# Kernel optimization log

Hardware: AMD Instinct MI355X
Metric: run time of the kernel (lower is better)

The kernel has to match this reference:

```python
import jax, jax.numpy as jnp
import numpy as np

T = 48  # top-T from init

def setup_inputs() -> dict:
    key = jax.random.key(0)
    ks = jax.random.split(key, 8)
    B, C, H, W = 16, 512, 32, 32
    tc = C // 8
    return {
        "x": jax.random.normal(ks[0], (B, C, H, W), jnp.float32),
        "fW": jax.random.normal(ks[1], (tc, C), jnp.float32) * 0.05,
        "fb": jax.random.normal(ks[2], (tc,), jnp.float32) * 0.05,
        "gW": jax.random.normal(ks[3], (tc, C), jnp.float32) * 0.05,
        "gb": jax.random.normal(ks[4], (tc,), jnp.float32) * 0.05,
        "hW": jax.random.normal(ks[5], (C, C), jnp.float32) * 0.05,
        "hb": jax.random.normal(ks[6], (C,), jnp.float32) * 0.05,
        "scale": jax.random.normal(ks[7], (1,), jnp.float32),
    }

def reference(x, fW, fb, gW, gb, hW, hb, scale):
    B, C, H, W = x.shape
    tc = fW.shape[0]
    HW = H * W
    # normalize by Frobenius norm over (batch, channel) -> [H, W]
    xn = x / jnp.linalg.norm(x, axis=(0, 1))[None, None]  # [B,C,H,W]
    # 1x1 convs, output already channel-last [B,H,W,out]
    f = jnp.einsum('bchw,oc->bhwo', xn, fW) + fb          # [B,H,W,tc]
    g = jnp.einsum('bchw,oc->bhwo', xn, gW) + gb          # [B,H,W,tc]
    h = jnp.einsum('bchw,oc->bhwo', xn, hW) + hb          # [B,H,W,C]
    xp = jnp.transpose(xn, (0, 2, 3, 1))                  # [B,H,W,C]
    # scores: queries H-major, keys W-major (faithful to permute(0,3,2,1).reshape)
    g_keys = jnp.transpose(g, (0, 3, 2, 1)).reshape(B, tc, HW)  # [B,tc,W*H]
    s = jnp.matmul(f.reshape(B, HW, tc), g_keys)          # [B,HW,HW]
    beta = jax.nn.softmax(s, axis=-1)
    o = jnp.matmul(beta, h.reshape(B, HW, C)).reshape(B, H, W, C)
    fdd = scale * o + xp                                  # [B,H,W,C]
    # per-batch correlation: fdd[b] ([H,W,C]) @ fdd[b].reshape(C,HW)
    corr = jnp.einsum('bhwc,bcn->bhwn', fdd, fdd.reshape(B, C, HW))  # [B,H,W,HW]
    top = jax.lax.top_k(corr, T)[0]                       # descending top-T values
    top = jax.nn.relu(top)
    top = top / jnp.linalg.norm(top, axis=(0, 1))[None, None]  # norm over (B,H) -> [W,T]
    return jnp.transpose(top, (0, 3, 1, 2))               # [B,T,H,W]
```

## Files before the change

### kernel.cpp

```cpp
#include <hip/hip_runtime.h>
#include <cstdint>
#include <cstddef>

#define B_   16
#define C_   512
#define H_   32
#define W_   32
#define HW_  1024
#define TC_  64
#define T_   48

typedef unsigned short u16;
typedef __attribute__((ext_vector_type(8))) short short8v;
typedef __attribute__((ext_vector_type(4))) float f32x4;

__device__ __forceinline__ u16 tobf(float x) {
    unsigned u = __float_as_uint(x);
    return (u16)((u + 0x7FFFu + ((u >> 16) & 1u)) >> 16);
}
__device__ __forceinline__ float frombf(u16 h) {
    return __uint_as_float(((unsigned)h) << 16);
}

__device__ __forceinline__ void gld16(const void* g, void* l) {
    __builtin_amdgcn_global_load_lds(
        (const __attribute__((address_space(1))) void*)g,
        (__attribute__((address_space(3))) void*)l, 16, 0, 0);
}

__global__ void k_colsq(const float* __restrict__ x, float* __restrict__ partial) {
    int bid = blockIdx.x;
    int col = (bid & 3) * 256 + threadIdx.x;
    int r0  = (bid >> 2) * 128;
    const float* p = x + (size_t)r0 * HW_ + col;
    float s = 0.f;
    for (int r = 0; r < 128; ++r) { float v = p[(size_t)r * HW_]; s += v * v; }
    partial[(size_t)(bid >> 2) * HW_ + col] = s;
}

__global__ void k_rsqrt(const float* __restrict__ partial, float* __restrict__ ninv) {
    int i = blockIdx.x * 256 + threadIdx.x;
    if (i < HW_) {
        float s = 0.f;
        for (int r = 0; r < 64; ++r) s += partial[(size_t)r * HW_ + i];
        ninv[i] = rsqrtf(s);
    }
}

__global__ void k_transpose(const float* __restrict__ x, const float* __restrict__ ninv,
                            u16* __restrict__ obH) {
    __shared__ float tile[32][33];
    int b  = blockIdx.z;
    int m0 = blockIdx.x * 32, c0 = blockIdx.y * 32;
    int tx = threadIdx.x, ty = threadIdx.y;
    const float* xb = x + (size_t)b * C_ * HW_;
    #pragma unroll
    for (int j = 0; j < 32; j += 8)
        tile[ty + j][tx] = xb[(size_t)(c0 + ty + j) * HW_ + m0 + tx];
    __syncthreads();
    size_t base = (size_t)b * HW_ * C_;
    #pragma unroll
    for (int j = 0; j < 32; j += 8) {
        int m = m0 + ty + j;
        obH[base + (size_t)m * C_ + c0 + tx] = tobf(tile[tx][ty + j] * ninv[m]);
    }
}

__global__ void k_packW(const float* __restrict__ in, u16* __restrict__ oh) {
    size_t i = (size_t)blockIdx.x * 256 + threadIdx.x;
    oh[i] = tobf(in[i]);
}
__global__ void k_packFG(const float* __restrict__ fW, const float* __restrict__ gW,
                         const float* __restrict__ fb, const float* __restrict__ gb,
                         u16* __restrict__ oh, float* __restrict__ fgb) {
    int idx = blockIdx.x * 256 + threadIdx.x;
    int row = idx >> 9, c = idx & 511;
    float v = (row < 64) ? fW[row * 512 + c] : gW[(row - 64) * 512 + c];
    oh[idx] = tobf(v);
    if (idx < 128) fgb[idx] = (idx < 64) ? fb[idx] : gb[idx - 64];
}

template<int PERMB, int EPI>
__global__ __launch_bounds__(256) void k_gemm1(
    const u16* __restrict__ A, const u16* __restrict__ Bm,
    const float* __restrict__ bias,
    float* __restrict__ Cf, u16* __restrict__ Ch,
    const float* __restrict__ scaleP,
    int N, int K, int lda, int ldb, long sA, long sB, long sC)
{
    __shared__ u16 lds[3 * 8192];
    const int b = blockIdx.z;
    const u16* pA = A + (size_t)b * sA;
    const u16* pB = Bm + (size_t)b * sB;
    const int m0 = blockIdx.y * 128, n0 = blockIdx.x * 128;
    const int tid = threadIdx.x, wave = tid >> 6, lane = tid & 63;
    const int wm = wave >> 1, wn = wave & 1;
    const int g = lane >> 4;

    f32x4 acc[4][4];
    #pragma unroll
    for (int i = 0; i < 4; ++i)
        #pragma unroll
        for (int j = 0; j < 4; ++j) { f32x4 z = {0.f,0.f,0.f,0.f}; acc[i][j] = z; }

    auto STAGE = [&](int kt, int buf) {
        const int k0 = kt << 5;
        u16* lb = lds + buf * 8192;
        #pragma unroll
        for (int q = 0; q < 4; ++q) {
            int ci = wave * 4 + q;
            bool isA = ci < 8;
            int li = ci & 7;
            const u16* gp = isA ? pA : pB;
            int ld = isA ? lda : ldb;
            int rb = isA ? m0 : n0;
            int rp = li * 8 + (lane >> 3);
            int gg = (lane & 7) ^ (rp & 7);
            int r  = rp * 2 + (gg >> 2);
            int kc = k0 + (gg & 3) * 8;
            int rowg = rb + r;
            if (PERMB && !isA) rowg = ((rowg & 31) << 5) | (rowg >> 5);
            gld16(gp + (size_t)rowg * ld + kc,
                  lb + (isA ? 0 : 4096) + li * 512 + lane * 8);
        }
    };
    auto COMPUTE = [&](int buf) {
        const u16* As = lds + buf * 8192;
        const u16* Bs = As + 4096;
        short8v av[4];
        #pragma unroll
        for (int i = 0; i < 4; ++i) {
            int r = wm * 64 + i * 16 + (lane & 15);
            int rp = r >> 1, gg = ((r & 1) << 2) + g;
            av[i] = *(const short8v*)(As + rp * 64 + ((gg ^ (rp & 7)) << 3));
        }
        #pragma unroll
        for (int j = 0; j < 4; ++j) {
            int r = wn * 64 + j * 16 + (lane & 15);
            int rp = r >> 1, gg = ((r & 1) << 2) + g;
            short8v bv = *(const short8v*)(Bs + rp * 64 + ((gg ^ (rp & 7)) << 3));
            #pragma unroll
            for (int i = 0; i < 4; ++i)
                acc[i][j] = __builtin_amdgcn_mfma_f32_16x16x32_bf16(av[i], bv, acc[i][j], 0, 0, 0);
        }
    };

    const int nkt = K >> 5;
    STAGE(0, 0);
    STAGE(1, 1);
    int cur = 0;
    for (int kt = 0; kt < nkt; ++kt) {
        int nxt2 = cur + 2; if (nxt2 >= 3) nxt2 -= 3;
        if (kt + 2 < nkt) {
            STAGE(kt + 2, nxt2);
            asm volatile("s_waitcnt vmcnt(8)" ::: "memory");
        } else if (kt + 1 < nkt) {
            asm volatile("s_waitcnt vmcnt(4)" ::: "memory");
        } else {
            asm volatile("s_waitcnt vmcnt(0)" ::: "memory");
        }
        __builtin_amdgcn_s_barrier();
        __builtin_amdgcn_sched_barrier(0);
        COMPUTE(cur);
        __builtin_amdgcn_sched_barrier(0);
        __builtin_amdgcn_s_barrier();
        ++cur; if (cur >= 3) cur -= 3;
    }

    const float sc = (EPI == 2) ? scaleP[0] : 0.f;
    const int colbase = n0 + wn * 64 + (lane & 15);
    const int rowbase = m0 + wm * 64 + ((lane >> 4) << 2);
    #pragma unroll
    for (int i = 0; i < 4; ++i)
        #pragma unroll
        for (int j = 0; j < 4; ++j) {
            int col = colbase + j * 16;
            #pragma unroll
            for (int rg = 0; rg < 4; ++rg) {
                int row = rowbase + i * 16 + rg;
                size_t idx = (size_t)b * sC + (size_t)row * N + col;
                float a = acc[i][j][rg];
                if (EPI == 0)      Cf[idx] = a;
                else if (EPI == 2) Ch[idx] = tobf(sc * a + frombf(Ch[idx]));
                else if (EPI == 4) Ch[idx] = tobf(a);
                else if (EPI == 5) Ch[idx] = tobf(a + bias[row]);
                else               Ch[idx] = tobf(a + bias[col]);
            }
        }
}

template<int PERMB, int EPI>
__global__ __launch_bounds__(512) void k_gemm2(
    const u16* __restrict__ A, const u16* __restrict__ Bm,
    const float* __restrict__ bias,
    float* __restrict__ Cf, u16* __restrict__ Ch,
    const float* __restrict__ scaleP,
    int N, int K, int lda, int ldb, long sA, long sB, long sC)
{
    __shared__ u16 lds[3 * 12288];
    const int b = blockIdx.z;
    const u16* pA = A + (size_t)b * sA;
    const u16* pB = Bm + (size_t)b * sB;
    const int m0 = blockIdx.y * 128, n0 = blockIdx.x * 256;
    const int tid = threadIdx.x, wave = tid >> 6, lane = tid & 63;
    const int wm = wave >> 2, wn = wave & 3;
    const int g = lane >> 4;

    f32x4 acc[4][4];
    #pragma unroll
    for (int i = 0; i < 4; ++i)
        #pragma unroll
        for (int j = 0; j < 4; ++j) { f32x4 z = {0.f,0.f,0.f,0.f}; acc[i][j] = z; }

    auto STAGE = [&](int kt, int buf) {
        const int k0 = kt << 5;
        u16* lb = lds + buf * 12288;
        #pragma unroll
        for (int q = 0; q < 3; ++q) {
            int ci = wave * 3 + q;
            bool isA = ci < 8;
            int li = isA ? ci : ci - 8;
            const u16* gp = isA ? pA : pB;
            int ld = isA ? lda : ldb;
            int rb = isA ? m0 : n0;
            int rp = li * 8 + (lane >> 3);
            int gg = (lane & 7) ^ (rp & 7);
            int r  = rp * 2 + (gg >> 2);
            int kc = k0 + (gg & 3) * 8;
            int rowg = rb + r;
            if (PERMB && !isA) rowg = ((rowg & 31) << 5) | (rowg >> 5);
            gld16(gp + (size_t)rowg * ld + kc,
                  lb + (isA ? 0 : 4096) + li * 512 + lane * 8);
        }
    };
    auto COMPUTE = [&](int buf) {
        const u16* As = lds + buf * 12288;
        const u16* Bs = As + 4096;
        short8v av[4];
        #pragma unroll
        for (int i = 0; i < 4; ++i) {
            int r = wm * 64 + i * 16 + (lane & 15);
            int rp = r >> 1, gg = ((r & 1) << 2) + g;
            av[i] = *(const short8v*)(As + rp * 64 + ((gg ^ (rp & 7)) << 3));
        }
        #pragma unroll
        for (int j = 0; j < 4; ++j) {
            int r = wn * 64 + j * 16 + (lane & 15);
            int rp = r >> 1, gg = ((r & 1) << 2) + g;
            short8v bv = *(const short8v*)(Bs + rp * 64 + ((gg ^ (rp & 7)) << 3));
            #pragma unroll
            for (int i = 0; i < 4; ++i)
                acc[i][j] = __builtin_amdgcn_mfma_f32_16x16x32_bf16(av[i], bv, acc[i][j], 0, 0, 0);
        }
    };

    const int nkt = K >> 5;
    STAGE(0, 0);
    STAGE(1, 1);
    int cur = 0;
    for (int kt = 0; kt < nkt; ++kt) {
        int nxt2 = cur + 2; if (nxt2 >= 3) nxt2 -= 3;
        if (kt + 2 < nkt) {
            STAGE(kt + 2, nxt2);
            asm volatile("s_waitcnt vmcnt(6)" ::: "memory");
        } else if (kt + 1 < nkt) {
            asm volatile("s_waitcnt vmcnt(3)" ::: "memory");
        } else {
            asm volatile("s_waitcnt vmcnt(0)" ::: "memory");
        }
        __builtin_amdgcn_s_barrier();
        __builtin_amdgcn_sched_barrier(0);
        COMPUTE(cur);
        __builtin_amdgcn_sched_barrier(0);
        __builtin_amdgcn_s_barrier();
        ++cur; if (cur >= 3) cur -= 3;
    }

    const float sc = (EPI == 2) ? scaleP[0] : 0.f;
    const int colbase = n0 + wn * 64 + (lane & 15);
    const int rowbase = m0 + wm * 64 + ((lane >> 4) << 2);
    #pragma unroll
    for (int i = 0; i < 4; ++i)
        #pragma unroll
        for (int j = 0; j < 4; ++j) {
            int col = colbase + j * 16;
            #pragma unroll
            for (int rg = 0; rg < 4; ++rg) {
                int row = rowbase + i * 16 + rg;
                size_t idx = (size_t)b * sC + (size_t)row * N + col;
                float a = acc[i][j][rg];
                if (EPI == 0)      Cf[idx] = a;
                else if (EPI == 2) Ch[idx] = tobf(sc * a + frombf(Ch[idx]));
                else if (EPI == 4) Ch[idx] = tobf(a);
                else if (EPI == 5) Ch[idx] = tobf(a + bias[row]);
                else               Ch[idx] = tobf(a + bias[col]);
            }
        }
}

__global__ __launch_bounds__(256) void k_softmax(u16* __restrict__ S) {
    size_t row = blockIdx.x;
    u16* r = S + row * (size_t)HW_;
    int t = threadIdx.x;
    ushort4 raw = ((const ushort4*)r)[t];
    float v0 = frombf(raw.x), v1 = frombf(raw.y), v2 = frombf(raw.z), v3 = frombf(raw.w);

    __shared__ float redm[4], reds[4];
    int wid = t >> 6, lane = t & 63;

    float m = fmaxf(fmaxf(v0, v1), fmaxf(v2, v3));
    for (int o = 32; o > 0; o >>= 1) m = fmaxf(m, __shfl_down(m, o));
    if (lane == 0) redm[wid] = m;
    __syncthreads();
    if (t == 0) redm[0] = fmaxf(fmaxf(redm[0], redm[1]), fmaxf(redm[2], redm[3]));
    __syncthreads();
    m = redm[0];

    v0 = expf(v0 - m); v1 = expf(v1 - m); v2 = expf(v2 - m); v3 = expf(v3 - m);
    float s = v0 + v1 + v2 + v3;
    for (int o = 32; o > 0; o >>= 1) s += __shfl_down(s, o);
    if (lane == 0) reds[wid] = s;
    __syncthreads();
    if (t == 0) reds[0] = reds[0] + reds[1] + reds[2] + reds[3];
    __syncthreads();
    float inv = 1.f / reds[0];
    ushort4 o4;
    o4.x = tobf(v0 * inv); o4.y = tobf(v1 * inv);
    o4.z = tobf(v2 * inv); o4.w = tobf(v3 * inv);
    ((ushort4*)r)[t] = o4;
}

__global__ void k_tposeU1(const u16* __restrict__ src, u16* __restrict__ dst) {
    __shared__ u16 tile[32][33];
    int b = blockIdx.z;
    const u16* sb = src + (size_t)b * (C_ * HW_);
    u16* db = dst + (size_t)b * (C_ * HW_);
    int c0 = blockIdx.x * 32, r0 = blockIdx.y * 32;
    int tx = threadIdx.x, ty = threadIdx.y;
    #pragma unroll
    for (int j = 0; j < 32; j += 8)
        tile[ty + j][tx] = sb[(size_t)(r0 + ty + j) * HW_ + c0 + tx];
    __syncthreads();
    #pragma unroll
    for (int j = 0; j < 32; j += 8)
        db[(size_t)(c0 + ty + j) * C_ + r0 + tx] = tile[tx][ty + j];
}

__device__ __forceinline__ float sort64_desc(float v, int lane) {
    #pragma unroll
    for (int k = 2; k <= 64; k <<= 1) {
        #pragma unroll
        for (int j = k >> 1; j > 0; j >>= 1) {
            float o = __shfl_xor(v, j);
            bool takeMax = (((lane & k) == 0) == ((lane & j) == 0));
            v = takeMax ? fmaxf(v, o) : fminf(v, o);
        }
    }
    return v;
}
__device__ __forceinline__ float bmerge64_desc(float a, float b, int lane) {
    float br = __shfl(b, 63 - lane);
    float c = fmaxf(a, br);
    #pragma unroll
    for (int j = 32; j > 0; j >>= 1) {
        float o = __shfl_xor(c, j);
        c = ((lane & j) == 0) ? fmaxf(c, o) : fminf(c, o);
    }
    return c;
}

__global__ __launch_bounds__(256) void k_topk(const float* __restrict__ corr,
                                              float* __restrict__ topv) {
    __shared__ float buf[4][1024];
    int wave = threadIdx.x >> 6, lane = threadIdx.x & 63;
    int row = blockIdx.x * 4 + wave;
    const float4* rp = (const float4*)(corr + (size_t)row * HW_);

    float4 e[4];
    #pragma unroll
    for (int q = 0; q < 4; ++q) e[q] = rp[lane * 4 + q];

    float gm = -INFINITY;
    #pragma unroll
    for (int q = 0; q < 4; ++q)
        gm = fmaxf(gm, fmaxf(fmaxf(e[q].x, e[q].y), fmaxf(e[q].z, e[q].w)));
    float sorted = sort64_desc(gm, lane);
    float tau = __shfl(sorted, T_ - 1);

    int c = 0;
    #pragma unroll
    for (int q = 0; q < 4; ++q)
        c += (e[q].x >= tau) + (e[q].y >= tau) + (e[q].z >= tau) + (e[q].w >= tau);
    int sc = c;
    #pragma unroll
    for (int o = 1; o < 64; o <<= 1) {
        int t2 = __shfl_up(sc, o);
        if (lane >= o) sc += t2;
    }
    int off = sc - c;
    int cnt = __shfl(sc, 63);

    float* wb = buf[wave];
    #pragma unroll
    for (int q = 0; q < 4; ++q) {
        if (e[q].x >= tau) wb[off++] = e[q].x;
        if (e[q].y >= tau) wb[off++] = e[q].y;
        if (e[q].z >= tau) wb[off++] = e[q].z;
        if (e[q].w >= tau) wb[off++] = e[q].w;
    }

    float* orow = topv + (size_t)row * T_;
    if (cnt <= 64) {
        float a = (lane < cnt) ? wb[lane] : -INFINITY;
        a = sort64_desc(a, lane);
        if (lane < T_) orow[lane] = fmaxf(a, 0.f);
    } else if (cnt <= 128) {
        float a  = sort64_desc(wb[lane], lane);
        float b2 = sort64_desc((lane < cnt - 64) ? wb[64 + lane] : -INFINITY, lane);
        float m2 = bmerge64_desc(a, b2, lane);
        if (lane < T_) orow[lane] = fmaxf(m2, 0.f);
    } else {
        int P = 256; while (P < cnt) P <<= 1;
        for (int i = cnt + lane; i < P; i += 64) wb[i] = -INFINITY;
        for (int k = 2; k <= P; k <<= 1)
            for (int j = k >> 1; j > 0; j >>= 1)
                for (int t2 = lane; t2 < P; t2 += 64) {
                    int ixj = t2 ^ j;
                    if (ixj > t2) {
                        float a = wb[t2], b3 = wb[ixj];
                        bool desc = ((t2 & k) == 0);
                        if (desc ? (a < b3) : (a > b3)) { wb[t2] = b3; wb[ixj] = a; }
                    }
                }
        if (lane < T_) orow[lane] = fmaxf(wb[lane], 0.f);
    }
}

__global__ void k_colss(const float* __restrict__ topv, float* __restrict__ colss) {
    int o = blockIdx.x;
    int w = o / T_, t = o % T_;
    int lane = threadIdx.x;
    float s = 0.f;
    for (int i = lane; i < 512; i += 64) {
        int b = i >> 5, h = i & 31;
        float v = topv[(size_t)((b << 10) + (h << 5) + w) * T_ + t];
        s += v * v;
    }
    for (int off = 32; off > 0; off >>= 1) s += __shfl_down(s, off);
    if (lane == 0) colss[o] = s;
}

__global__ void k_final(const float* __restrict__ topv, const float* __restrict__ colss,
                        float* __restrict__ out) {
    int idx = blockIdx.x * 256 + threadIdx.x;
    if (idx >= B_ * T_ * HW_) return;
    int w = idx & 31;
    int h = (idx >> 5) & 31;
    int t = (idx >> 10) % T_;
    int b = idx / (T_ * HW_);
    float v = topv[(size_t)((b << 10) + (h << 5) + w) * T_ + t];
    out[idx] = v * rsqrtf(colss[w * T_ + t]);
}

extern "C" void kernel_launch(void* const* d_in, const int* in_sizes, int n_in,
                              void* d_out, int out_size, void* d_ws, size_t ws_size,
                              hipStream_t stream) {
    const float* x     = (const float*)d_in[0];
    const float* fW    = (const float*)d_in[1];
    const float* fb    = (const float*)d_in[2];
    const float* gW    = (const float*)d_in[3];
    const float* gb    = (const float*)d_in[4];
    const float* hW    = (const float*)d_in[5];
    const float* hb    = (const float*)d_in[6];
    const float* scale = (const float*)d_in[7];
    float* out = (float*)d_out;

    char* wsb = (char*)d_ws;
    float* part = (float*)(wsb + 0);
    float* ninv = (float*)(wsb + 262144);
    u16*   hWh  = (u16*)(wsb + 266240);
    u16*   fgWh = (u16*)(wsb + 790528);
    float* fgb  = (float*)(wsb + 921600);
    u16*   xnH  = (u16*)(wsb + 922112);
    u16*   fgH  = (u16*)(wsb + 17699328);
    u16*   fgL  = (u16*)(wsb + 21893632);
    u16*   hvTH = (u16*)(wsb + 26087936);
    float* S    = (float*)(wsb + 42865152);
    float* topv = (float*)fgH;
    float* colss= (float*)fgL;
    u16*   Sp   = (u16*)S;

    const long sXn = 524288;
    const long sFG = 131072;
    const long sS  = 1048576;

    k_colsq<<<256, 256, 0, stream>>>(x, part);
    k_rsqrt<<<4, 256, 0, stream>>>(part, ninv);

    k_transpose<<<dim3(32, 16, 16), dim3(32, 8), 0, stream>>>(x, ninv, xnH);

    k_packW<<<1024, 256, 0, stream>>>(hW, hWh);
    k_packFG<<<256, 256, 0, stream>>>(fW, gW, fb, gb, fgWh, fgb);

    k_gemm1<0, 6><<<dim3(1, 8, 16), 256, 0, stream>>>(
        xnH, fgWh, fgb, nullptr, fgH, nullptr,
        128, 512, 512, 512, sXn, 0, sFG);

    k_gemm1<0, 5><<<dim3(8, 4, 16), 256, 0, stream>>>(
        hWh, xnH, hb, nullptr, hvTH, nullptr,
        1024, 512, 512, 512, 0, sXn, sXn);

    k_gemm2<1, 4><<<dim3(4, 8, 16), 512, 0, stream>>>(
        fgH, fgH + 64, nullptr, nullptr, Sp, nullptr,
        1024, 64, 128, 128, sFG, sFG, sS);

    k_softmax<<<B_ * HW_, 256, 0, stream>>>(Sp);

    k_gemm1<0, 2><<<dim3(4, 8, 16), 256, 0, stream>>>(
        Sp, hvTH, nullptr, nullptr, xnH, scale,
        512, 1024, 1024, 1024, sS, sXn, sXn);

    k_tposeU1<<<dim3(32, 16, 16), dim3(32, 8), 0, stream>>>(xnH, hvTH);

    k_gemm1<0, 0><<<dim3(8, 8, 16), 256, 0, stream>>>(
        xnH, hvTH, nullptr, S, nullptr, nullptr,
        1024, 512, 512, 512, sXn, sXn, sS);

    k_topk<<<B_ * HW_ / 4, 256, 0, stream>>>(S, topv);

    k_colss<<<W_ * T_, 64, 0, stream>>>(topv, colss);
    k_final<<<(B_ * T_ * HW_ + 255) / 256, 256, 0, stream>>>(topv, colss, out);
}
```

Before: 215.4 us.

## Fuse score GEMM with row softmax and swizzle GEMM block order

Replaces the separate score GEMM plus softmax kernel with one kernel. Each block computes a 64x1024 tile of scores with MFMA, does the row max and sum reductions in registers and shared memory, and writes normalized bf16 probabilities through a swizzled LDS staging buffer. This removes the bf16 score round trip to global memory and one launch. The score logits are also no longer rounded to bf16 before softmax. Separately, k_gemm1 remaps block IDs in a stride-8 interleave, likely meant to spread blocks across XCDs and improve cache locality. The fused kernel uses about 136KB of LDS, which caps occupancy at one block per CU.

```diff
diff --git a/kernel.cpp b/kernel.cpp
--- a/kernel.cpp
+++ b/kernel.cpp
@@ -80,7 +80,7 @@
     if (idx < 128) fgb[idx] = (idx < 64) ? fb[idx] : gb[idx - 64];
 }
 
-template<int PERMB, int EPI>
+template<int EPI>
 __global__ __launch_bounds__(256) void k_gemm1(
     const u16* __restrict__ A, const u16* __restrict__ Bm,
     const float* __restrict__ bias,
@@ -89,10 +89,18 @@
     int N, int K, int lda, int ldb, long sA, long sB, long sC)
 {
     __shared__ u16 lds[3 * 8192];
-    const int b = blockIdx.z;
+    const int gx = gridDim.x, gy = gridDim.y, gz = gridDim.z;
+    int bidl = blockIdx.x + gx * (blockIdx.y + gy * blockIdx.z);
+    int nwg = gx * gy * gz;
+    int sw = (bidl & 7) * (nwg >> 3) + (bidl >> 3);
+    int gxy = gx * gy;
+    int bz = sw / gxy, rem = sw - bz * gxy;
+    int by = rem / gx, bx = rem - by * gx;
+
+    const int b = bz;
     const u16* pA = A + (size_t)b * sA;
     const u16* pB = Bm + (size_t)b * sB;
-    const int m0 = blockIdx.y * 128, n0 = blockIdx.x * 128;
+    const int m0 = by * 128, n0 = bx * 128;
     const int tid = threadIdx.x, wave = tid >> 6, lane = tid & 63;
     const int wm = wave >> 1, wn = wave & 1;
     const int g = lane >> 4;
@@ -118,9 +126,7 @@
             int gg = (lane & 7) ^ (rp & 7);
             int r  = rp * 2 + (gg >> 2);
             int kc = k0 + (gg & 3) * 8;
-            int rowg = rb + r;
-            if (PERMB && !isA) rowg = ((rowg & 31) << 5) | (rowg >> 5);
-            gld16(gp + (size_t)rowg * ld + kc,
+            gld16(gp + (size_t)(rb + r) * ld + kc,
                   lb + (isA ? 0 : 4096) + li * 512 + lane * 8);
         }
     };
@@ -182,152 +188,175 @@
                 float a = acc[i][j][rg];
                 if (EPI == 0)      Cf[idx] = a;
                 else if (EPI == 2) Ch[idx] = tobf(sc * a + frombf(Ch[idx]));
-                else if (EPI == 4) Ch[idx] = tobf(a);
                 else if (EPI == 5) Ch[idx] = tobf(a + bias[row]);
                 else               Ch[idx] = tobf(a + bias[col]);
             }
         }
 }
 
-template<int PERMB, int EPI>
-__global__ __launch_bounds__(512) void k_gemm2(
-    const u16* __restrict__ A, const u16* __restrict__ Bm,
-    const float* __restrict__ bias,
-    float* __restrict__ Cf, u16* __restrict__ Ch,
-    const float* __restrict__ scaleP,
-    int N, int K, int lda, int ldb, long sA, long sB, long sC)
+__global__ __launch_bounds__(512) void k_ssoft(
+    const u16* __restrict__ fg,
+    u16* __restrict__ P)
 {
-    __shared__ u16 lds[3 * 12288];
-    const int b = blockIdx.z;
-    const u16* pA = A + (size_t)b * sA;
-    const u16* pB = Bm + (size_t)b * sB;
-    const int m0 = blockIdx.y * 128, n0 = blockIdx.x * 256;
+    __shared__ u16 lds[69632];
+    __shared__ float red[512];
+    __shared__ float rowm[64];
+    __shared__ float rinv[64];
+
+    const int b = blockIdx.y;
+    const int m0 = blockIdx.x * 64;
+    const u16* fgb = fg + (size_t)b * 131072;
     const int tid = threadIdx.x, wave = tid >> 6, lane = tid & 63;
-    const int wm = wave >> 2, wn = wave & 3;
+    const int wn = wave;
     const int g = lane >> 4;
 
-    f32x4 acc[4][4];
-    #pragma unroll
-    for (int i = 0; i < 4; ++i)
-        #pragma unroll
-        for (int j = 0; j < 4; ++j) { f32x4 z = {0.f,0.f,0.f,0.f}; acc[i][j] = z; }
-
-    auto STAGE = [&](int kt, int buf) {
-        const int k0 = kt << 5;
-        u16* lb = lds + buf * 12288;
-        #pragma unroll
-        for (int q = 0; q < 3; ++q) {
-            int ci = wave * 3 + q;
-            bool isA = ci < 8;
-            int li = isA ? ci : ci - 8;
-            const u16* gp = isA ? pA : pB;
-            int ld = isA ? lda : ldb;
-            int rb = isA ? m0 : n0;
+    #pragma unroll
+    for (int kc = 0; kc < 2; ++kc) {
+        #pragma unroll
+        for (int q = 0; q < 8; ++q) {
+            int li = wave * 8 + q;
             int rp = li * 8 + (lane >> 3);
             int gg = (lane & 7) ^ (rp & 7);
             int r  = rp * 2 + (gg >> 2);
-            int kc = k0 + (gg & 3) * 8;
-            int rowg = rb + r;
-            if (PERMB && !isA) rowg = ((rowg & 31) << 5) | (rowg >> 5);
-            gld16(gp + (size_t)rowg * ld + kc,
-                  lb + (isA ? 0 : 4096) + li * 512 + lane * 8);
-        }
-    };
-    auto COMPUTE = [&](int buf) {
-        const u16* As = lds + buf * 12288;
-        const u16* Bs = As + 4096;
+            int n2 = ((r & 31) << 5) | (r >> 5);
+            int kcol = 64 + kc * 32 + (gg & 3) * 8;
+            gld16(fgb + (size_t)n2 * 128 + kcol,
+                  lds + 4096 + kc * 32768 + li * 512 + lane * 8);
+        }
+        if (lane < 32) {
+            int rp = wave * 4 + (lane >> 3);
+            int gg = (lane & 7) ^ (rp & 7);
+            int r  = rp * 2 + (gg >> 2);
+            int kcol = kc * 32 + (gg & 3) * 8;
+            gld16(fgb + (size_t)(m0 + r) * 128 + kcol,
+                  lds + kc * 2048 + wave * 256 + lane * 8);
+        }
+    }
+    __syncthreads();
+
+    f32x4 acc[4][8];
+    #pragma unroll
+    for (int i = 0; i < 4; ++i)
+        #pragma unroll
+        for (int j = 0; j < 8; ++j) { f32x4 z = {0.f,0.f,0.f,0.f}; acc[i][j] = z; }
+
+    #pragma unroll
+    for (int kc = 0; kc < 2; ++kc) {
+        const u16* As = lds + kc * 2048;
+        const u16* Bs = lds + 4096 + kc * 32768;
         short8v av[4];
         #pragma unroll
         for (int i = 0; i < 4; ++i) {
-            int r = wm * 64 + i * 16 + (lane & 15);
+            int r = i * 16 + (lane & 15);
             int rp = r >> 1, gg = ((r & 1) << 2) + g;
             av[i] = *(const short8v*)(As + rp * 64 + ((gg ^ (rp & 7)) << 3));
         }
         #pragma unroll
-        for (int j = 0; j < 4; ++j) {
-            int r = wn * 64 + j * 16 + (lane & 15);
-            int rp = r >> 1, gg = ((r & 1) << 2) + g;
+        for (int j = 0; j < 8; ++j) {
+            int n = wn * 128 + j * 16 + (lane & 15);
+            int rp = n >> 1, gg = ((n & 1) << 2) + g;
             short8v bv = *(const short8v*)(Bs + rp * 64 + ((gg ^ (rp & 7)) << 3));
             #pragma unroll
             for (int i = 0; i < 4; ++i)
                 acc[i][j] = __builtin_amdgcn_mfma_f32_16x16x32_bf16(av[i], bv, acc[i][j], 0, 0, 0);
         }
-    };
-
-    const int nkt = K >> 5;
-    STAGE(0, 0);
-    STAGE(1, 1);
-    int cur = 0;
-    for (int kt = 0; kt < nkt; ++kt) {
-        int nxt2 = cur + 2; if (nxt2 >= 3) nxt2 -= 3;
-        if (kt + 2 < nkt) {
-            STAGE(kt + 2, nxt2);
-            asm volatile("s_waitcnt vmcnt(6)" ::: "memory");
-        } else if (kt + 1 < nkt) {
-            asm volatile("s_waitcnt vmcnt(3)" ::: "memory");
-        } else {
-            asm volatile("s_waitcnt vmcnt(0)" ::: "memory");
-        }
-        __builtin_amdgcn_s_barrier();
-        __builtin_amdgcn_sched_barrier(0);
-        COMPUTE(cur);
-        __builtin_amdgcn_sched_barrier(0);
-        __builtin_amdgcn_s_barrier();
-        ++cur; if (cur >= 3) cur -= 3;
-    }
-
-    const float sc = (EPI == 2) ? scaleP[0] : 0.f;
-    const int colbase = n0 + wn * 64 + (lane & 15);
-    const int rowbase = m0 + wm * 64 + ((lane >> 4) << 2);
+    }
+
+    const int rgrp = (lane >> 4) << 2;
+    float pm[4][4];
     #pragma unroll
     for (int i = 0; i < 4; ++i)
         #pragma unroll
-        for (int j = 0; j < 4; ++j) {
-            int col = colbase + j * 16;
-            #pragma unroll
-            for (int rg = 0; rg < 4; ++rg) {
-                int row = rowbase + i * 16 + rg;
-                size_t idx = (size_t)b * sC + (size_t)row * N + col;
-                float a = acc[i][j][rg];
-                if (EPI == 0)      Cf[idx] = a;
-                else if (EPI == 2) Ch[idx] = tobf(sc * a + frombf(Ch[idx]));
-                else if (EPI == 4) Ch[idx] = tobf(a);
-                else if (EPI == 5) Ch[idx] = tobf(a + bias[row]);
-                else               Ch[idx] = tobf(a + bias[col]);
+        for (int rg = 0; rg < 4; ++rg) {
+            float m = acc[i][0][rg];
+            #pragma unroll
+            for (int j = 1; j < 8; ++j) m = fmaxf(m, acc[i][j][rg]);
+            pm[i][rg] = m;
+        }
+    #pragma unroll
+    for (int o = 1; o < 16; o <<= 1)
+        #pragma unroll
+        for (int i = 0; i < 4; ++i)
+            #pragma unroll
+            for (int rg = 0; rg < 4; ++rg)
+                pm[i][rg] = fmaxf(pm[i][rg], __shfl_xor(pm[i][rg], o));
+    if ((lane & 15) == 0)
+        #pragma unroll
+        for (int i = 0; i < 4; ++i)
+            #pragma unroll
+            for (int rg = 0; rg < 4; ++rg)
+                red[wn * 64 + i * 16 + rgrp + rg] = pm[i][rg];
+    __syncthreads();
+    if (tid < 64) {
+        float m = red[tid];
+        #pragma unroll
+        for (int w = 1; w < 8; ++w) m = fmaxf(m, red[w * 64 + tid]);
+        rowm[tid] = m;
+    }
+    __syncthreads();
+
+    float ps[4][4];
+    #pragma unroll
+    for (int i = 0; i < 4; ++i)
+        #pragma unroll
+        for (int rg = 0; rg < 4; ++rg) {
+            float m = rowm[i * 16 + rgrp + rg];
+            float s = 0.f;
+            #pragma unroll
+            for (int j = 0; j < 8; ++j) {
+                float e = expf(acc[i][j][rg] - m);
+                acc[i][j][rg] = e;
+                s += e;
             }
-        }
-}
-
-__global__ __launch_bounds__(256) void k_softmax(u16* __restrict__ S) {
-    size_t row = blockIdx.x;
-    u16* r = S + row * (size_t)HW_;
-    int t = threadIdx.x;
-    ushort4 raw = ((const ushort4*)r)[t];
-    float v0 = frombf(raw.x), v1 = frombf(raw.y), v2 = frombf(raw.z), v3 = frombf(raw.w);
-
-    __shared__ float redm[4], reds[4];
-    int wid = t >> 6, lane = t & 63;
-
-    float m = fmaxf(fmaxf(v0, v1), fmaxf(v2, v3));
-    for (int o = 32; o > 0; o >>= 1) m = fmaxf(m, __shfl_down(m, o));
-    if (lane == 0) redm[wid] = m;
-    __syncthreads();
-    if (t == 0) redm[0] = fmaxf(fmaxf(redm[0], redm[1]), fmaxf(redm[2], redm[3]));
-    __syncthreads();
-    m = redm[0];
-
-    v0 = expf(v0 - m); v1 = expf(v1 - m); v2 = expf(v2 - m); v3 = expf(v3 - m);
-    float s = v0 + v1 + v2 + v3;
-    for (int o = 32; o > 0; o >>= 1) s += __shfl_down(s, o);
-    if (lane == 0) reds[wid] = s;
-    __syncthreads();
-    if (t == 0) reds[0] = reds[0] + reds[1] + reds[2] + reds[3];
-    __syncthreads();
-    float inv = 1.f / reds[0];
-    ushort4 o4;
-    o4.x = tobf(v0 * inv); o4.y = tobf(v1 * inv);
-    o4.z = tobf(v2 * inv); o4.w = tobf(v3 * inv);
-    ((ushort4*)r)[t] = o4;
+            ps[i][rg] = s;
+        }
+    #pragma unroll
+    for (int o = 1; o < 16; o <<= 1)
+        #pragma unroll
+        for (int i = 0; i < 4; ++i)
+            #pragma unroll
+            for (int rg = 0; rg < 4; ++rg)
+                ps[i][rg] += __shfl_xor(ps[i][rg], o);
+    if ((lane & 15) == 0)
+        #pragma unroll
+        for (int i = 0; i < 4; ++i)
+            #pragma unroll
+            for (int rg = 0; rg < 4; ++rg)
+                red[wn * 64 + i * 16 + rgrp + rg] = ps[i][rg];
+    __syncthreads();
+    if (tid < 64) {
+        float s = red[tid];
+        #pragma unroll
+        for (int w = 1; w < 8; ++w) s += red[w * 64 + tid];
+        rinv[tid] = 1.f / s;
+    }
+    __syncthreads();
+
+    u16* Plds = lds + 4096;
+    #pragma unroll
+    for (int i = 0; i < 4; ++i)
+        #pragma unroll
+        for (int rg = 0; rg < 4; ++rg) {
+            int r = i * 16 + rgrp + rg;
+            float riv = rinv[r];
+            int sx = (r & 7) << 4;
+            #pragma unroll
+            for (int j = 0; j < 8; ++j) {
+                u16 v = tobf(acc[i][j][rg] * riv);
+                int col = wn * 128 + ((j * 16) ^ sx) + (lane & 15);
+                Plds[r * 1024 + col] = v;
+            }
+        }
+    __syncthreads();
+
+    for (int it = 0; it < 16; ++it) {
+        int r  = it * 4 + (tid >> 7);
+        int cb = (tid & 127) * 8;
+        int sx = (r & 7) << 4;
+        int src = r * 1024 + (cb & ~127) + ((cb & 127) ^ sx);
+        short8v v = *(const short8v*)(Plds + src);
+        *(short8v*)(P + ((size_t)b * HW_ + m0 + r) * (size_t)HW_ + cb) = v;
+    }
 }
 
 __global__ void k_tposeU1(const u16* __restrict__ src, u16* __restrict__ dst) {
@@ -502,27 +531,23 @@
     k_packW<<<1024, 256, 0, stream>>>(hW, hWh);
     k_packFG<<<256, 256, 0, stream>>>(fW, gW, fb, gb, fgWh, fgb);
 
-    k_gemm1<0, 6><<<dim3(1, 8, 16), 256, 0, stream>>>(
+    k_gemm1<6><<<dim3(1, 8, 16), 256, 0, stream>>>(
         xnH, fgWh, fgb, nullptr, fgH, nullptr,
         128, 512, 512, 512, sXn, 0, sFG);
 
-    k_gemm1<0, 5><<<dim3(8, 4, 16), 256, 0, stream>>>(
+    k_gemm1<5><<<dim3(8, 4, 16), 256, 0, stream>>>(
         hWh, xnH, hb, nullptr, hvTH, nullptr,
         1024, 512, 512, 512, 0, sXn, sXn);
 
-    k_gemm2<1, 4><<<dim3(4, 8, 16), 512, 0, stream>>>(
-        fgH, fgH + 64, nullptr, nullptr, Sp, nullptr,
-        1024, 64, 128, 128, sFG, sFG, sS);
-
-    k_softmax<<<B_ * HW_, 256, 0, stream>>>(Sp);
-
-    k_gemm1<0, 2><<<dim3(4, 8, 16), 256, 0, stream>>>(
+    k_ssoft<<<dim3(16, 16), 512, 0, stream>>>(fgH, Sp);
+
+    k_gemm1<2><<<dim3(4, 8, 16), 256, 0, stream>>>(
         Sp, hvTH, nullptr, nullptr, xnH, scale,
         512, 1024, 1024, 1024, sS, sXn, sXn);
 
     k_tposeU1<<<dim3(32, 16, 16), dim3(32, 8), 0, stream>>>(xnH, hvTH);
 
-    k_gemm1<0, 0><<<dim3(8, 8, 16), 256, 0, stream>>>(
+    k_gemm1<0><<<dim3(8, 8, 16), 256, 0, stream>>>(
         xnH, hvTH, nullptr, S, nullptr, nullptr,
         1024, 512, 512, 512, sXn, sXn, sS);
 
```

Result: faster. 195.4 us (-9.3%).
